# Optimization experiments

Measured on AMD Instinct MI355X. Metric: run time of the kernel, lower is better.

The kernel has to match this reference:

```python
import jax, jax.numpy as jnp
import numpy as np

MAX_SPAN = 255
EPS = 1e-5
B, L, C = 4, 1024, 512
DK, DV, H = 512, 1024, 8
DKH, DVH = DK // H, DV // H


def _bn(x, gamma, beta, axes):
    # Training-mode batch norm: normalize over `axes` per channel.
    m = jnp.mean(x, axis=axes, keepdims=True)
    v = jnp.var(x, axis=axes, keepdims=True)
    return gamma * (x - m) * jax.lax.rsqrt(v + EPS) + beta


def _rel_index(length):
    # distance_matrix[l, m] = m - l + MAX_SPAN - 1, clamped to table range.
    ki = jnp.arange(length)
    d = ki[None, :] - ki[:, None] + (MAX_SPAN - 1)
    return jnp.clip(d, 0, 2 * MAX_SPAN - 2)


def setup_inputs() -> dict:
    key = jax.random.key(0)
    ks = jax.random.split(key, 6)
    std_qkv = DK ** (-0.5)
    return {
        "x": jax.random.normal(ks[0], (B, L, C), jnp.float32),
        "W_qkv": jax.random.normal(ks[1], (C, 2 * DK + DV), jnp.float32) * std_qkv,
        "bn_qkv_gamma": jnp.ones((2 * DK + DV,), jnp.float32),
        "bn_qkv_beta": jnp.zeros((2 * DK + DV,), jnp.float32),
        "bn_sim_gamma": jnp.ones((3, H), jnp.float32),
        "bn_sim_beta": jnp.zeros((3, H), jnp.float32),
        "bn_out_gamma": jnp.ones((2, H, DVH), jnp.float32),
        "bn_out_beta": jnp.zeros((2, H, DVH), jnp.float32),
        "emb_q_rpe": jax.random.normal(ks[2], (2 * MAX_SPAN - 1, DKH), jnp.float32),
        "emb_k_rpe": jax.random.normal(ks[3], (2 * MAX_SPAN - 1, DKH), jnp.float32),
        "emb_v_rpe": jax.random.normal(ks[4], (2 * MAX_SPAN - 1, DVH), jnp.float32),
    }


def reference(x, W_qkv, bn_qkv_gamma, bn_qkv_beta, bn_sim_gamma, bn_sim_beta,
              bn_out_gamma, bn_out_beta, emb_q_rpe, emb_k_rpe, emb_v_rpe):
    b, l, c = x.shape
    rel = _rel_index(l)                                # [L, M] int indices

    qkv = jnp.einsum('blc,cd->bld', x, W_qkv)
    qkv = _bn(qkv, bn_qkv_gamma, bn_qkv_beta, axes=(0, 1))
    q, k, v = jnp.split(qkv, [DK, 2 * DK], axis=-1)
    q = q.reshape(b, l, H, DKH).transpose(0, 2, 1, 3)  # [B,H,L,dk]
    k = k.reshape(b, l, H, DKH).transpose(0, 2, 1, 3)  # [B,H,M,dk]
    v = v.reshape(b, l, H, DVH)                        # [B,M,H,dv]

    q_rpe = emb_q_rpe[rel]                             # [L,M,dk]
    k_rpe = emb_k_rpe[rel]                             # [L,M,dk]
    v_rpe = emb_v_rpe[rel]                             # [L,M,dv]

    sims = jnp.stack([
        jnp.einsum('bhld,bhmd->bhlm', q, k),           # content
        jnp.einsum('bhld,lmd->bhlm', q, q_rpe),        # query rpe
        jnp.einsum('bhmd,lmd->bhlm', k, k_rpe),        # key rpe
    ])                                                 # [3,B,H,L,M]
    sims = _bn(sims, bn_sim_gamma[:, None, :, None, None],
               bn_sim_beta[:, None, :, None, None], axes=(1, 3, 4))
    logits = jnp.sum(sims, axis=0)                     # [B,H,L,M]
    weights = jax.nn.softmax(logits, axis=-1)

    retrieved = jnp.stack([
        jnp.einsum('bhlm,bmhd->bhld', weights, v),     # content
        jnp.einsum('bhlm,lmd->bhld', weights, v_rpe),  # rpe
    ])                                                 # [2,B,H,L,dv]
    retrieved = _bn(retrieved, bn_out_gamma[:, None, :, None, :],
                    bn_out_beta[:, None, :, None, :], axes=(1, 3))
    out = jnp.sum(retrieved, axis=0)                   # [B,H,L,dv]
    out = out.transpose(0, 2, 1, 3).reshape(b, l, DV)
    return out
```

## Files before the change

kernel.cpp:

```cpp
#include <hip/hip_runtime.h>


#define EPSN 1e-5f

#define NWS_QKV   0ul
#define NWS_S     8388608ul
#define NWS_G1    25165824ul
#define NWS_G2    33554432ul
#define NWS_RET   41943040ul
#define NWS_STATS 50331648ul
#define NWS_COLSUM (NWS_STATS)
#define NWS_COLSQ  (NWS_STATS + 2048)
#define NWS_SIMSUM (NWS_STATS + 4096)
#define NWS_SIMSQ  (NWS_STATS + 4120)
#define NWS_OUTSUM (NWS_STATS + 4144)
#define NWS_OUTSQ  (NWS_STATS + 6192)
#define NWS_STATS_N 8240ul
#define NWS_FOLD   (NWS_STATS + NWS_STATS_N)
#define NWS_QSCALE (NWS_FOLD)
#define NWS_QSHIFT (NWS_FOLD + 2048)
#define NWS_SIMA   (NWS_FOLD + 4096)
#define NWS_SIMC   (NWS_FOLD + 4120)
#define NWS_TOTAL_FLOATS (NWS_FOLD + 4128ul)

#define NWS_XHI (NWS_RET)
#define NWS_XLO (NWS_RET + 1048576ul)
#define NWS_WTH (NWS_RET + 2097152ul)
#define NWS_WTL (NWS_RET + 2621440ul)
#define NWS_VB  (NWS_G1)
#define NWS_EVB (NWS_G2)

typedef __attribute__((ext_vector_type(8))) short short8v;
typedef __attribute__((ext_vector_type(4))) float float4v;

__device__ __forceinline__ unsigned short f2bf(float x) {
    union { float f; unsigned int u; } c; c.f = x;
    unsigned int u = c.u + 0x7fffu + ((c.u >> 16) & 1u);
    return (unsigned short)(u >> 16);
}
__device__ __forceinline__ float bf2f(unsigned short x) {
    union { unsigned int u; float f; } c; c.u = ((unsigned int)x) << 16;
    return c.f;
}

__global__ __launch_bounds__(256) void k_prepx(const float* __restrict__ x,
                                               unsigned short* __restrict__ xh,
                                               unsigned short* __restrict__ xl) {
    const size_t e = ((size_t)blockIdx.x * 256 + threadIdx.x) * 8;
    unsigned short th[8], tl[8];
    #pragma unroll
    for (int i = 0; i < 2; ++i) {
        float4 v = *(const float4*)(x + e + i * 4);
        float vv[4] = {v.x, v.y, v.z, v.w};
        #pragma unroll
        for (int j = 0; j < 4; ++j) {
            unsigned short hi = f2bf(vv[j]);
            th[i*4+j] = hi;
            tl[i*4+j] = f2bf(vv[j] - bf2f(hi));
        }
    }
    *(uint4*)(xh + e) = *(uint4*)th;
    *(uint4*)(xl + e) = *(uint4*)tl;
}

__global__ __launch_bounds__(256) void k_prepw(const float* __restrict__ w,
                                               unsigned short* __restrict__ wth,
                                               unsigned short* __restrict__ wtl) {
    __shared__ float ws[64][68];
    const int t = threadIdx.x;
    const int n0 = blockIdx.x * 64;
    const int k0 = blockIdx.y * 64;
    #pragma unroll
    for (int i = 0; i < 4; ++i) {
        int row = (t >> 4) + i * 16;
        int col = (t & 15) * 4;
        float4 v = *(const float4*)(w + (size_t)(k0 + row) * 2048 + n0 + col);
        ws[row][col] = v.x; ws[row][col+1] = v.y; ws[row][col+2] = v.z; ws[row][col+3] = v.w;
    }
    __syncthreads();
    const int n = t >> 2;
    const int kc = (t & 3) * 16;
    unsigned short th[16], tl[16];
    #pragma unroll
    for (int j = 0; j < 16; ++j) {
        float v = ws[kc + j][n];
        unsigned short hi = f2bf(v);
        th[j] = hi; tl[j] = f2bf(v - bf2f(hi));
    }
    size_t base = (size_t)(n0 + n) * 512 + k0 + kc;
    *(uint4*)(wth + base) = *(uint4*)&th[0];
    *(uint4*)(wth + base + 8) = *(uint4*)&th[8];
    *(uint4*)(wtl + base) = *(uint4*)&tl[0];
    *(uint4*)(wtl + base + 8) = *(uint4*)&tl[8];
}

__global__ __launch_bounds__(256) void k_gemm_qkv2(
        const unsigned short* __restrict__ xh, const unsigned short* __restrict__ xl,
        const unsigned short* __restrict__ wth, const unsigned short* __restrict__ wtl,
        float* __restrict__ qkv) {
    __shared__ unsigned short Ah[4096], Al[4096], Bh[4096], Bl[4096];
    const int t = threadIdx.x;
    const int lane = t & 63, w = t >> 6;
    const int n0 = blockIdx.x * 64;
    const int m0 = blockIdx.y * 64;
    const int sr = t >> 2, sc = (t & 3) * 16;
    const int x0 = (sc * 2) ^ ((sr & 7) << 4);
    const int x1 = ((sc * 2) + 16) ^ ((sr & 7) << 4);
    const int fr = lane & 15, kg = lane >> 4;

    float4v acc[4];
    #pragma unroll
    for (int nt = 0; nt < 4; ++nt) { acc[nt][0]=0.f; acc[nt][1]=0.f; acc[nt][2]=0.f; acc[nt][3]=0.f; }

    for (int k0 = 0; k0 < 512; k0 += 64) {
        __syncthreads();
        {
            size_t a = (size_t)(m0 + sr) * 512 + k0 + sc;
            uint4 va0 = *(const uint4*)(xh + a), va1 = *(const uint4*)(xh + a + 8);
            *(uint4*)((char*)Ah + sr * 128 + x0) = va0;
            *(uint4*)((char*)Ah + sr * 128 + x1) = va1;
            uint4 vb0 = *(const uint4*)(xl + a), vb1 = *(const uint4*)(xl + a + 8);
            *(uint4*)((char*)Al + sr * 128 + x0) = vb0;
            *(uint4*)((char*)Al + sr * 128 + x1) = vb1;
            size_t bâ = (size_t)(n0 + sr) * 512 + k0 + sc;
            uint4 vc0 = *(const uint4*)(wth + bâ), vc1 = *(const uint4*)(wth + bâ + 8);
            *(uint4*)((char*)Bh + sr * 128 + x0) = vc0;
            *(uint4*)((char*)Bh + sr * 128 + x1) = vc1;
            uint4 vd0 = *(const uint4*)(wtl + bâ), vd1 = *(const uint4*)(wtl + bâ + 8);
            *(uint4*)((char*)Bl + sr * 128 + x0) = vd0;
            *(uint4*)((char*)Bl + sr * 128 + x1) = vd1;
        }
        __syncthreads();
        #pragma unroll
        for (int ks = 0; ks < 2; ++ks) {
            int arow = w * 16 + fr;
            int aoff = (kg * 16 + ks * 64) ^ ((arow & 7) << 4);
            short8v ah = *(short8v*)((char*)Ah + arow * 128 + aoff);
            short8v al = *(short8v*)((char*)Al + arow * 128 + aoff);
            #pragma unroll
            for (int nt = 0; nt < 4; ++nt) {
                int brow = nt * 16 + fr;
                int boff = (kg * 16 + ks * 64) ^ ((brow & 7) << 4);
                short8v bh = *(short8v*)((char*)Bh + brow * 128 + boff);
                short8v bl = *(short8v*)((char*)Bl + brow * 128 + boff);
                acc[nt] = __builtin_amdgcn_mfma_f32_16x16x32_bf16(ah, bh, acc[nt], 0, 0, 0);
                acc[nt] = __builtin_amdgcn_mfma_f32_16x16x32_bf16(ah, bl, acc[nt], 0, 0, 0);
                acc[nt] = __builtin_amdgcn_mfma_f32_16x16x32_bf16(al, bh, acc[nt], 0, 0, 0);
            }
        }
    }
    const int crow = (lane >> 4) * 4, ccol = lane & 15;
    #pragma unroll
    for (int nt = 0; nt < 4; ++nt)
        #pragma unroll
        for (int j = 0; j < 4; ++j)
            qkv[(size_t)(m0 + w * 16 + crow + j) * 2048 + n0 + nt * 16 + ccol] = acc[nt][j];
}

__global__ __launch_bounds__(256) void k_colstats(const float* __restrict__ src,
                                                  float* __restrict__ sum,
                                                  float* __restrict__ sq) {
    const int ch = blockIdx.x * 256 + threadIdx.x;
    const int r0 = blockIdx.y * 256;
    float s = 0.f, q = 0.f;
    for (int r = 0; r < 256; ++r) {
        float v = src[(size_t)(r0 + r) * 2048 + ch];
        s += v; q += v * v;
    }
    atomicAdd(&sum[ch], s);
    atomicAdd(&sq[ch], q);
}

__global__ __launch_bounds__(256) void k_fold_qkv(const float* __restrict__ sum,
                                                  const float* __restrict__ sq,
                                                  const float* __restrict__ gamma,
                                                  const float* __restrict__ beta,
                                                  float* __restrict__ scale,
                                                  float* __restrict__ shift) {
    const int ch = blockIdx.x * 256 + threadIdx.x;
    float m = sum[ch] * (1.f / 4096.f);
    float v = sq[ch] * (1.f / 4096.f) - m * m;
    float sc = gamma[ch] * rsqrtf(v + EPSN);
    scale[ch] = sc;
    shift[ch] = beta[ch] - sc * m;
}

__global__ void k_fold_sim(const float* __restrict__ simsum,
                           const float* __restrict__ simsq,
                           const float* __restrict__ gamma,
                           const float* __restrict__ beta,
                           float* __restrict__ a_out,
                           float* __restrict__ c_out) {
    __shared__ float part[24];
    const int t = threadIdx.x;
    const float inv = 1.f / (4.f * 1024.f * 1024.f);
    if (t < 24) {
        float m = simsum[t] * inv;
        float v = simsq[t] * inv - m * m;
        float a = gamma[t] * rsqrtf(v + EPSN);
        a_out[t] = a;
        part[t] = beta[t] - a * m;
    }
    __syncthreads();
    if (t < 8) c_out[t] = part[t] + part[8 + t] + part[16 + t];
}

__device__ __forceinline__ float g_mult(int WHICH, int row, int r) {
    int c0, c508, rlo, rhi;
    if (WHICH == 1) {
        c0 = row - 253 > 0 ? row - 253 : 0;
        c508 = 770 - row > 0 ? 770 - row : 0;
        rlo = 254 - row > 1 ? 254 - row : 1;
        rhi = 1277 - row < 507 ? 1277 - row : 507;
    } else {
        c0 = 770 - row > 0 ? 770 - row : 0;
        c508 = row - 253 > 0 ? row - 253 : 0;
        rlo = row - 769 > 1 ? row - 769 : 1;
        rhi = row + 254 < 507 ? row + 254 : 507;
    }
    return (r == 0) ? (float)c0
         : (r == 508) ? (float)c508
         : (r >= rlo && r <= rhi) ? 1.f : 0.f;
}

template<int GM>
__global__ __launch_bounds__(256) void k_gemm_bt(
        const float* __restrict__ qkv,
        const float* __restrict__ qscale, const float* __restrict__ qshift,
        const float* __restrict__ emb,
        unsigned short* __restrict__ outp,
        float* __restrict__ simsum, float* __restrict__ simsq) {
    __shared__ unsigned short Ab[64 * 64];
    __shared__ unsigned short Bb[64 * 64];
    const int t = threadIdx.x;
    const int lane = t & 63, w = t >> 6;
    const int n0 = blockIdx.x * 64;
    const int m0 = blockIdx.y * 64;
    const int z  = blockIdx.z;
    const int sr = t >> 2, sc = (t & 3) * 16;

    {
        int grow = m0 + sr;
        const float* src; int ch;
        if (GM == 0) {
            int b = z >> 3, h = z & 7;
            ch = h * 64 + sc;
            src = qkv + ((size_t)(b * 1024 + grow)) * 2048 + ch;
        } else {
            int zz = grow >> 10, l = grow & 1023;
            int b = zz >> 3, h = zz & 7;
            ch = (GM == 2 ? 512 : 0) + h * 64 + sc;
            src = qkv + ((size_t)(b * 1024 + l)) * 2048 + ch;
        }
        unsigned short tmp[16];
        #pragma unroll
        for (int i = 0; i < 4; ++i) {
            float4 v  = *(const float4*)(src + i * 4);
            float4 s4 = *(const float4*)(qscale + ch + i * 4);
            float4 h4 = *(const float4*)(qshift + ch + i * 4);
            tmp[i*4+0] = f2bf(v.x*s4.x+h4.x); tmp[i*4+1] = f2bf(v.y*s4.y+h4.y);
            tmp[i*4+2] = f2bf(v.z*s4.z+h4.z); tmp[i*4+3] = f2bf(v.w*s4.w+h4.w);
        }
        int x0 = (sc * 2) ^ ((sr & 7) << 4);
        int x1 = ((sc * 2) + 16) ^ ((sr & 7) << 4);
        *(uint4*)((char*)Ab + sr * 128 + x0) = *(uint4*)&tmp[0];
        *(uint4*)((char*)Ab + sr * 128 + x1) = *(uint4*)&tmp[8];
    }
    {
        unsigned short tmp[16];
        if (GM == 0) {
            int b = z >> 3, h = z & 7;
            int ch = 512 + h * 64 + sc;
            const float* src = qkv + ((size_t)(b * 1024 + n0 + sr)) * 2048 + ch;
            #pragma unroll
            for (int i = 0; i < 4; ++i) {
                float4 v  = *(const float4*)(src + i * 4);
                float4 s4 = *(const float4*)(qscale + ch + i * 4);
                float4 h4 = *(const float4*)(qshift + ch + i * 4);
                tmp[i*4+0] = f2bf(v.x*s4.x+h4.x); tmp[i*4+1] = f2bf(v.y*s4.y+h4.y);
                tmp[i*4+2] = f2bf(v.z*s4.z+h4.z); tmp[i*4+3] = f2bf(v.w*s4.w+h4.w);
            }
        } else {
            int r = n0 + sr;
            if (r < 509) {
                const float* src = emb + (size_t)r * 64 + sc;
                #pragma unroll
                for (int i = 0; i < 4; ++i) {
                    float4 v = *(const float4*)(src + i * 4);
                    tmp[i*4+0] = f2bf(v.x); tmp[i*4+1] = f2bf(v.y);
                    tmp[i*4+2] = f2bf(v.z); tmp[i*4+3] = f2bf(v.w);
                }
            } else {
                #pragma unroll
                for (int i = 0; i < 16; ++i) tmp[i] = 0;
            }
        }
        int x0 = (sc * 2) ^ ((sr & 7) << 4);
        int x1 = ((sc * 2) + 16) ^ ((sr & 7) << 4);
        *(uint4*)((char*)Bb + sr * 128 + x0) = *(uint4*)&tmp[0];
        *(uint4*)((char*)Bb + sr * 128 + x1) = *(uint4*)&tmp[8];
    }
    __syncthreads();

    const int fr = lane & 15, kg = lane >> 4;
    float4v acc[4];
    #pragma unroll
    for (int nt = 0; nt < 4; ++nt) { acc[nt][0]=0.f; acc[nt][1]=0.f; acc[nt][2]=0.f; acc[nt][3]=0.f; }
    #pragma unroll
    for (int ks = 0; ks < 2; ++ks) {
        int arow = w * 16 + fr;
        short8v a = *(short8v*)((char*)Ab + arow * 128 +
                                ((kg * 16 + ks * 64) ^ ((arow & 7) << 4)));
        #pragma unroll
        for (int nt = 0; nt < 4; ++nt) {
            int brow = nt * 16 + fr;
            short8v bf = *(short8v*)((char*)Bb + brow * 128 +
                                     ((kg * 16 + ks * 64) ^ ((brow & 7) << 4)));
            acc[nt] = __builtin_amdgcn_mfma_f32_16x16x32_bf16(a, bf, acc[nt], 0, 0, 0);
        }
    }

    const int crow = (lane >> 4) * 4;
    const int ccol = lane & 15;
    size_t base; int ldc;
    if (GM == 0) { base = (((size_t)z * 1024) + m0 + w * 16) * 1024 + n0; ldc = 1024; }
    else         { base = ((size_t)(m0 + w * 16)) * 512 + n0;             ldc = 512;  }
    #pragma unroll
    for (int nt = 0; nt < 4; ++nt)
        #pragma unroll
        for (int j = 0; j < 4; ++j)
            outp[base + (size_t)(crow + j) * ldc + nt * 16 + ccol] = f2bf(acc[nt][j]);

    float s = 0.f, q = 0.f;
    #pragma unroll
    for (int nt = 0; nt < 4; ++nt)
        #pragma unroll
        for (int j = 0; j < 4; ++j) {
            float v = acc[nt][j];
            float mlt;
            if (GM == 0) mlt = 1.f;
            else {
                int row = (m0 + w * 16 + crow + j) & 1023;
                int r = n0 + nt * 16 + ccol;
                mlt = g_mult(GM, row, r);
            }
            s += mlt * v; q += mlt * v * v;
        }
    #pragma unroll
    for (int off = 32; off; off >>= 1) { s += __shfl_xor(s, off); q += __shfl_xor(q, off); }
    __syncthreads();
    float* red = (float*)Ab;
    if (lane == 0) { red[w * 2] = s; red[w * 2 + 1] = q; }
    __syncthreads();
    if (t == 0) {
        float s4 = red[0] + red[2] + red[4] + red[6];
        float q4 = red[1] + red[3] + red[5] + red[7];
        int h = (GM == 0) ? (z & 7) : (((m0 >> 10)) & 7);
        int off0 = (GM == 0) ? 0 : (GM == 1 ? 8 : 16);
        atomicAdd(&simsum[off0 + h], s4);
        atomicAdd(&simsq[off0 + h], q4);
    }
}

__global__ __launch_bounds__(256) void k_logits(
        unsigned short* __restrict__ Sg,
        const unsigned short* __restrict__ G1g,
        const unsigned short* __restrict__ G2g,
        const float* __restrict__ sim_a) {
    const int t = threadIdx.x;
    const int l = blockIdx.x;
    const int z = blockIdx.y;
    const int h = z & 7;
    const float a0c = sim_a[h], a1c = sim_a[8 + h], a2c = sim_a[16 + h];
    const size_t zS = (size_t)z << 20;
    const size_t zG = (size_t)z * 524288;
    const int m = t * 4;
    unsigned short* sp = Sg + zS + (size_t)l * 1024 + m;
    uint2 sv = *(const uint2*)sp;
    const unsigned short* s16 = (const unsigned short*)&sv;
    const unsigned short* g1r = G1g + zG + (size_t)l * 512;
    unsigned short o16[4];
    #pragma unroll
    for (int j = 0; j < 4; ++j) {
        int r = m + j - l + 254;
        int rc = r < 0 ? 0 : (r > 508 ? 508 : r);
        float g1 = bf2f(g1r[rc]);
        float g2 = bf2f(G2g[zG + (size_t)(m + j) * 512 + rc]);
        float lg = a0c * bf2f(s16[j]) + a1c * g1 + a2c * g2;
        o16[j] = f2bf(lg);
    }
    *(uint2*)sp = *(uint2*)o16;
}

__global__ __launch_bounds__(256) void k_prepv(const float* __restrict__ qkv,
                                               const float* __restrict__ qscale,
                                               const float* __restrict__ qshift,
                                               unsigned short* __restrict__ vb) {
    const int row = blockIdx.x;
    const int ch = threadIdx.x * 4;
    float4 v  = *(const float4*)(qkv + (size_t)row * 2048 + 1024 + ch);
    float4 s4 = *(const float4*)(qscale + 1024 + ch);
    float4 h4 = *(const float4*)(qshift + 1024 + ch);
    unsigned short o[4];
    o[0] = f2bf(v.x*s4.x+h4.x); o[1] = f2bf(v.y*s4.y+h4.y);
    o[2] = f2bf(v.z*s4.z+h4.z); o[3] = f2bf(v.w*s4.w+h4.w);
    *(uint2*)(vb + (size_t)row * 1024 + ch) = *(uint2*)o;
}

__global__ __launch_bounds__(256) void k_prepev(const float* __restrict__ ev,
                                                unsigned short* __restrict__ evb) {
    const int e = blockIdx.x * 256 + threadIdx.x;
    const int r = e >> 7, d = e & 127;
    evb[e] = (r < 509) ? f2bf(ev[(size_t)r * 128 + d]) : (unsigned short)0;
}

#define W3_Ws 0
#define W3_Wr 1152
#define W3_V  9472

__global__ __launch_bounds__(256, 4) void k_attn4(
        const unsigned short* __restrict__ Lg,
        const unsigned short* __restrict__ Vb,
        const unsigned short* __restrict__ EVb,
        float* __restrict__ ret) {
    __shared__ unsigned short su[17920];
    const int t = threadIdx.x;
    const int lane = t & 63, wid = t >> 6;
    const int blk = blockIdx.x;
    const int lt = blk & 63;
    const int h  = (blk >> 6) & 7;
    const int b  = blk >> 9;
    const int l0 = lt * 16;
    const int z  = b * 8 + h;
    const size_t zS = (size_t)z << 20;

    {
        unsigned int* wz = (unsigned int*)(su + W3_Wr);
        #pragma unroll
        for (int i = 0; i < 17; ++i) { int idx = t + i * 256; if (idx < 4160) wz[idx] = 0u; }
    }
    float D[4]  = {0.f, 0.f, 0.f, 0.f};
    float e0[4] = {0.f, 0.f, 0.f, 0.f};
    float e1[4] = {0.f, 0.f, 0.f, 0.f};
    float4v accA0, accA1;
    accA0[0]=0.f; accA0[1]=0.f; accA0[2]=0.f; accA0[3]=0.f;
    accA1[0]=0.f; accA1[1]=0.f; accA1[2]=0.f; accA1[3]=0.f;

    const int vm = t >> 2, vd0 = (t & 3) * 32;
    const int fr = lane & 15, kg = lane >> 4;
    const int dbase = wid * 32;
    const size_t vbase = ((size_t)b * 1024) * 1024 + h * 128;

    for (int mt = 0; mt < 16; ++mt) {
        const int m0 = mt * 64;
        __syncthreads();
        uint4 vld[4];
        {
            const unsigned short* src = Vb + vbase + (size_t)(m0 + vm) * 1024 + vd0;
            vld[0] = *(const uint4*)(src);
            vld[1] = *(const uint4*)(src + 8);
            vld[2] = *(const uint4*)(src + 16);
            vld[3] = *(const uint4*)(src + 24);
        }
        #pragma unroll
        for (int rr = 0; rr < 4; ++rr) {
            const int lrow = wid * 4 + rr;
            const int l_g = l0 + lrow;
            const int r = m0 + lane - l_g + 254;
            float wv = __expf(bf2f(Lg[zS + (size_t)l_g * 1024 + m0 + lane]));
            D[rr] += wv;
            bool lo = r <= 0, hi = r >= 508;
            e0[rr] += lo ? wv : 0.f;
            e1[rr] += hi ? wv : 0.f;
            unsigned short hw = f2bf(wv);
            su[W3_Ws + lrow * 72 + lane] = hw;
            if (!lo && !hi) su[W3_Wr + lrow * 520 + r] = hw;
        }
        {
            unsigned short* dst = su + W3_V + vm * 132 + vd0;
            const uint2* vsrc = (const uint2*)vld;
            #pragma unroll
            for (int i = 0; i < 8; ++i) *(uint2*)(dst + i * 4) = vsrc[i];
        }
        __syncthreads();
        #pragma unroll
        for (int ks = 0; ks < 2; ++ks) {
            short8v af = *(const short8v*)(su + W3_Ws + fr * 72 + ks * 32 + kg * 8);
            #pragma unroll
            for (int nt = 0; nt < 2; ++nt) {
                const int d = dbase + nt * 16 + fr;
                const unsigned short* vp = su + W3_V + (ks * 32 + kg * 8) * 132 + d;
                short8v bf;
                bf[0] = (short)vp[0 * 132]; bf[1] = (short)vp[1 * 132];
                bf[2] = (short)vp[2 * 132]; bf[3] = (short)vp[3 * 132];
                bf[4] = (short)vp[4 * 132]; bf[5] = (short)vp[5 * 132];
                bf[6] = (short)vp[6 * 132]; bf[7] = (short)vp[7 * 132];
                if (nt == 0) accA0 = __builtin_amdgcn_mfma_f32_16x16x32_bf16(af, bf, accA0, 0, 0, 0);
                else         accA1 = __builtin_amdgcn_mfma_f32_16x16x32_bf16(af, bf, accA1, 0, 0, 0);
            }
        }
    }

    #pragma unroll
    for (int rr = 0; rr < 4; ++rr) {
        #pragma unroll
        for (int off = 32; off; off >>= 1) {
            D[rr]  += __shfl_xor(D[rr], off);
            e0[rr] += __shfl_xor(e0[rr], off);
            e1[rr] += __shfl_xor(e1[rr], off);
        }
    }
    float* Df = (float*)su;
    __syncthreads();
    if (lane == 0) {
        #pragma unroll
        for (int rr = 0; rr < 4; ++rr) {
            int lrow = wid * 4 + rr;
            Df[lrow] = D[rr];
            su[W3_Wr + lrow * 520 + 0]   = f2bf(e0[rr]);
            su[W3_Wr + lrow * 520 + 508] = f2bf(e1[rr]);
        }
    }
    __syncthreads();

    const int crow = (lane >> 4) * 4, ccol = lane & 15;
    {
        size_t rb = (((size_t)b * 8 + h) * 1024 + l0) * 128;
        #pragma unroll
        for (int j = 0; j < 4; ++j) {
            int row = crow + j;
            float dinv = 1.f / Df[row];
            ret[rb + (size_t)row * 128 + dbase + ccol]      = accA0[j] * dinv;
            ret[rb + (size_t)row * 128 + dbase + 16 + ccol] = accA1[j] * dinv;
        }
    }

    float4v accR0, accR1;
    accR0[0]=0.f; accR0[1]=0.f; accR0[2]=0.f; accR0[3]=0.f;
    accR1[0]=0.f; accR1[1]=0.f; accR1[2]=0.f; accR1[3]=0.f;
    for (int rc = 0; rc < 8; ++rc) {
        __syncthreads();
        {
            const unsigned short* src = EVb + (size_t)(rc * 64 + vm) * 128 + vd0;
            unsigned short* dst = su + W3_V + vm * 132 + vd0;
            uint4 a0 = *(const uint4*)(src);
            uint4 a1 = *(const uint4*)(src + 8);
            uint4 a2 = *(const uint4*)(src + 16);
            uint4 a3 = *(const uint4*)(src + 24);
            uint4 tmp[4] = {a0, a1, a2, a3};
            const uint2* vsrc = (const uint2*)tmp;
            #pragma unroll
            for (int i = 0; i < 8; ++i) *(uint2*)(dst + i * 4) = vsrc[i];
        }
        __syncthreads();
        #pragma unroll
        for (int ks = 0; ks < 2; ++ks) {
            short8v af = *(const short8v*)(su + W3_Wr + fr * 520 + rc * 64 + ks * 32 + kg * 8);
            #pragma unroll
            for (int nt = 0; nt < 2; ++nt) {
                const int d = dbase + nt * 16 + fr;
                const unsigned short* vp = su + W3_V + (ks * 32 + kg * 8) * 132 + d;
                short8v bf;
                bf[0] = (short)vp[0 * 132]; bf[1] = (short)vp[1 * 132];
                bf[2] = (short)vp[2 * 132]; bf[3] = (short)vp[3 * 132];
                bf[4] = (short)vp[4 * 132]; bf[5] = (short)vp[5 * 132];
                bf[6] = (short)vp[6 * 132]; bf[7] = (short)vp[7 * 132];
                if (nt == 0) accR0 = __builtin_amdgcn_mfma_f32_16x16x32_bf16(af, bf, accR0, 0, 0, 0);
                else         accR1 = __builtin_amdgcn_mfma_f32_16x16x32_bf16(af, bf, accR1, 0, 0, 0);
            }
        }
    }
    {
        size_t rb = ((((size_t)1 * 4 + b) * 8 + h) * 1024 + l0) * 128;
        #pragma unroll
        for (int j = 0; j < 4; ++j) {
            int row = crow + j;
            float dinv = 1.f / Df[row];
            ret[rb + (size_t)row * 128 + dbase + ccol]      = accR0[j] * dinv;
            ret[rb + (size_t)row * 128 + dbase + 16 + ccol] = accR1[j] * dinv;
        }
    }
}

__global__ __launch_bounds__(256) void k_outstats(const float* __restrict__ ret,
                                                  float* __restrict__ sum,
                                                  float* __restrict__ sq) {
    const int ch = blockIdx.x * 256 + threadIdx.x;
    const int s = ch >> 10, hd = ch & 1023;
    const int h = hd >> 7, d = hd & 127;
    const int row0 = blockIdx.y * 256;
    float sm_ = 0.f, q = 0.f;
    for (int r = 0; r < 256; ++r) {
        int row = row0 + r;
        int b = row >> 10, l = row & 1023;
        float v = ret[((((size_t)s * 4 + b) * 8 + h) * 1024 + l) * 128 + d];
        sm_ += v; q += v * v;
    }
    atomicAdd(&sum[ch], sm_);
    atomicAdd(&sq[ch], q);
}

__global__ __launch_bounds__(256) void k_final(const float* __restrict__ ret,
                                               const float* __restrict__ osum,
                                               const float* __restrict__ osq,
                                               const float* __restrict__ gamma,
                                               const float* __restrict__ beta,
                                               float* __restrict__ out) {
    const int idx = blockIdx.x * 256 + threadIdx.x;
    const int o = idx * 4;
    const int d = o & 127;
    const int h = (o >> 7) & 7;
    const int l = (o >> 10) & 1023;
    const int b = o >> 20;
    const int ch0 = h * 128 + d;
    const int ch1 = 1024 + ch0;
    float4 r0 = *(const float4*)(ret + ((((size_t)0 * 4 + b) * 8 + h) * 1024 + l) * 128 + d);
    float4 r1 = *(const float4*)(ret + ((((size_t)1 * 4 + b) * 8 + h) * 1024 + l) * 128 + d);
    float4 s0 = *(const float4*)(osum + ch0), q0 = *(const float4*)(osq + ch0);
    float4 s1 = *(const float4*)(osum + ch1), q1 = *(const float4*)(osq + ch1);
    float4 g0 = *(const float4*)(gamma + ch0), b0 = *(const float4*)(beta + ch0);
    float4 g1 = *(const float4*)(gamma + ch1), b1 = *(const float4*)(beta + ch1);
    const float inv = 1.f / 4096.f;
    float4 res;
    {
        float m0 = s0.x*inv, v0 = q0.x*inv - m0*m0, a0 = g0.x*rsqrtf(v0+EPSN);
        float m1 = s1.x*inv, v1 = q1.x*inv - m1*m1, a1 = g1.x*rsqrtf(v1+EPSN);
        res.x = a0*(r0.x-m0)+b0.x + a1*(r1.x-m1)+b1.x;
    }
    {
        float m0 = s0.y*inv, v0 = q0.y*inv - m0*m0, a0 = g0.y*rsqrtf(v0+EPSN);
        float m1 = s1.y*inv, v1 = q1.y*inv - m1*m1, a1 = g1.y*rsqrtf(v1+EPSN);
        res.y = a0*(r0.y-m0)+b0.y + a1*(r1.y-m1)+b1.y;
    }
    {
        float m0 = s0.z*inv, v0 = q0.z*inv - m0*m0, a0 = g0.z*rsqrtf(v0+EPSN);
        float m1 = s1.z*inv, v1 = q1.z*inv - m1*m1, a1 = g1.z*rsqrtf(v1+EPSN);
        res.z = a0*(r0.z-m0)+b0.z + a1*(r1.z-m1)+b1.z;
    }
    {
        float m0 = s0.w*inv, v0 = q0.w*inv - m0*m0, a0 = g0.w*rsqrtf(v0+EPSN);
        float m1 = s1.w*inv, v1 = q1.w*inv - m1*m1, a1 = g1.w*rsqrtf(v1+EPSN);
        res.w = a0*(r0.w-m0)+b0.w + a1*(r1.w-m1)+b1.w;
    }
    *(float4*)(out + o) = res;
}

extern "C" void kernel_launch(void* const* d_in, const int* in_sizes, int n_in,
                              void* d_out, int out_size, void* d_ws, size_t ws_size,
                              hipStream_t stream) {
    const float* x     = (const float*)d_in[0];
    const float* wqkv  = (const float*)d_in[1];
    const float* g_qkv = (const float*)d_in[2];
    const float* b_qkv = (const float*)d_in[3];
    const float* g_sim = (const float*)d_in[4];
    const float* b_sim = (const float*)d_in[5];
    const float* g_out = (const float*)d_in[6];
    const float* b_out = (const float*)d_in[7];
    const float* eq    = (const float*)d_in[8];
    const float* ek    = (const float*)d_in[9];
    const float* ev    = (const float*)d_in[10];
    float* ws  = (float*)d_ws;
    float* out = (float*)d_out;

    if (ws_size < NWS_TOTAL_FLOATS * sizeof(float)) {
        hipMemsetAsync(out, 0, (size_t)out_size * sizeof(float), stream);
        return;
    }

    float* qkv    = ws + NWS_QKV;
    unsigned short* Sg  = (unsigned short*)(ws + NWS_S);
    unsigned short* G1g = (unsigned short*)(ws + NWS_G1);
    unsigned short* G2g = (unsigned short*)(ws + NWS_G2);
    float* ret    = ws + NWS_RET;
    float* colsum = ws + NWS_COLSUM;
    float* colsq  = ws + NWS_COLSQ;
    float* simsum = ws + NWS_SIMSUM;
    float* simsq  = ws + NWS_SIMSQ;
    float* outsum = ws + NWS_OUTSUM;
    float* outsq  = ws + NWS_OUTSQ;
    float* qscale = ws + NWS_QSCALE;
    float* qshift = ws + NWS_QSHIFT;
    float* sim_a  = ws + NWS_SIMA;
    float* sim_c  = ws + NWS_SIMC;
    unsigned short* xh  = (unsigned short*)(ws + NWS_XHI);
    unsigned short* xl  = (unsigned short*)(ws + NWS_XLO);
    unsigned short* wth = (unsigned short*)(ws + NWS_WTH);
    unsigned short* wtl = (unsigned short*)(ws + NWS_WTL);
    unsigned short* vb  = (unsigned short*)(ws + NWS_VB);
    unsigned short* evb = (unsigned short*)(ws + NWS_EVB);
    (void)sim_c;

    hipMemsetAsync(ws + NWS_STATS, 0, NWS_STATS_N * sizeof(float), stream);

    k_prepx<<<dim3(1024), 256, 0, stream>>>(x, xh, xl);
    k_prepw<<<dim3(32, 8), 256, 0, stream>>>(wqkv, wth, wtl);
    k_gemm_qkv2<<<dim3(32, 64), 256, 0, stream>>>(xh, xl, wth, wtl, qkv);

    k_colstats<<<dim3(8, 16), 256, 0, stream>>>(qkv, colsum, colsq);
    k_fold_qkv<<<dim3(8), 256, 0, stream>>>(colsum, colsq, g_qkv, b_qkv, qscale, qshift);

    k_gemm_bt<0><<<dim3(16, 16, 32), 256, 0, stream>>>(qkv, qscale, qshift, eq, Sg, simsum, simsq);
    k_gemm_bt<1><<<dim3(8, 512, 1), 256, 0, stream>>>(qkv, qscale, qshift, eq, G1g, simsum, simsq);
    k_gemm_bt<2><<<dim3(8, 512, 1), 256, 0, stream>>>(qkv, qscale, qshift, ek, G2g, simsum, simsq);

    k_fold_sim<<<dim3(1), 32, 0, stream>>>(simsum, simsq, g_sim, b_sim, sim_a, ws + NWS_SIMC);

    k_logits<<<dim3(1024, 32), 256, 0, stream>>>(Sg, G1g, G2g, sim_a);

    k_prepv<<<dim3(4096), 256, 0, stream>>>(qkv, qscale, qshift, vb);
    k_prepev<<<dim3(256), 256, 0, stream>>>(ev, evb);

    k_attn4<<<dim3(2048), 256, 0, stream>>>(Sg, vb, evb, ret);

    k_outstats<<<dim3(8, 16), 256, 0, stream>>>(ret, outsum, outsq);
    k_final<<<dim3(4096), 256, 0, stream>>>(ret, outsum, outsq, g_out, b_out, out);
}
```

Baseline: 656.0 us.

## Fuse logits combination into attention kernel and pre-transpose V operands

```diff
diff --git a/kernel.cpp b/kernel.cpp
--- a/kernel.cpp
+++ b/kernel.cpp
@@ -27,8 +27,6 @@
 #define NWS_XLO (NWS_RET + 1048576ul)
 #define NWS_WTH (NWS_RET + 2097152ul)
 #define NWS_WTL (NWS_RET + 2621440ul)
-#define NWS_VB  (NWS_G1)
-#define NWS_EVB (NWS_G2)
 
 typedef __attribute__((ext_vector_type(8))) short short8v;
 typedef __attribute__((ext_vector_type(4))) float float4v;
@@ -116,19 +114,15 @@
         __syncthreads();
         {
             size_t a = (size_t)(m0 + sr) * 512 + k0 + sc;
-            uint4 va0 = *(const uint4*)(xh + a), va1 = *(const uint4*)(xh + a + 8);
-            *(uint4*)((char*)Ah + sr * 128 + x0) = va0;
-            *(uint4*)((char*)Ah + sr * 128 + x1) = va1;
-            uint4 vb0 = *(const uint4*)(xl + a), vb1 = *(const uint4*)(xl + a + 8);
-            *(uint4*)((char*)Al + sr * 128 + x0) = vb0;
-            *(uint4*)((char*)Al + sr * 128 + x1) = vb1;
-            size_t bâ = (size_t)(n0 + sr) * 512 + k0 + sc;
-            uint4 vc0 = *(const uint4*)(wth + bâ), vc1 = *(const uint4*)(wth + bâ + 8);
-            *(uint4*)((char*)Bh + sr * 128 + x0) = vc0;
-            *(uint4*)((char*)Bh + sr * 128 + x1) = vc1;
-            uint4 vd0 = *(const uint4*)(wtl + bâ), vd1 = *(const uint4*)(wtl + bâ + 8);
-            *(uint4*)((char*)Bl + sr * 128 + x0) = vd0;
-            *(uint4*)((char*)Bl + sr * 128 + x1) = vd1;
+            *(uint4*)((char*)Ah + sr * 128 + x0) = *(const uint4*)(xh + a);
+            *(uint4*)((char*)Ah + sr * 128 + x1) = *(const uint4*)(xh + a + 8);
+            *(uint4*)((char*)Al + sr * 128 + x0) = *(const uint4*)(xl + a);
+            *(uint4*)((char*)Al + sr * 128 + x1) = *(const uint4*)(xl + a + 8);
+            size_t bb = (size_t)(n0 + sr) * 512 + k0 + sc;
+            *(uint4*)((char*)Bh + sr * 128 + x0) = *(const uint4*)(wth + bb);
+            *(uint4*)((char*)Bh + sr * 128 + x1) = *(const uint4*)(wth + bb + 8);
+            *(uint4*)((char*)Bl + sr * 128 + x0) = *(const uint4*)(wtl + bb);
+            *(uint4*)((char*)Bl + sr * 128 + x1) = *(const uint4*)(wtl + bb + 8);
         }
         __syncthreads();
         #pragma unroll
@@ -203,6 +197,87 @@
     }
     __syncthreads();
     if (t < 8) c_out[t] = part[t] + part[8 + t] + part[16 + t];
+}
+
+__global__ __launch_bounds__(256) void k_prepvT(const float* __restrict__ qkv,
+                                                const float* __restrict__ qscale,
+                                                const float* __restrict__ qshift,
+                                                unsigned short* __restrict__ vbT) {
+    __shared__ unsigned short tb[64 * 130];
+    const int t = threadIdx.x;
+    const int blk = blockIdx.x;
+    const int z = blk >> 4, mt = blk & 15;
+    const int b = z >> 3, h = z & 7;
+    const int m0 = mt * 64;
+    {
+        const int m = t >> 2, dg = (t & 3) * 32;
+        const int ch = 1024 + h * 128 + dg;
+        const float* src = qkv + ((size_t)(b * 1024 + m0 + m)) * 2048 + ch;
+        const float* scp = qscale + ch;
+        const float* shp = qshift + ch;
+        unsigned short* dst = tb + m * 130 + dg;
+        #pragma unroll
+        for (int i = 0; i < 8; ++i) {
+            float4 v  = *(const float4*)(src + i * 4);
+            float4 s4 = *(const float4*)(scp + i * 4);
+            float4 h4 = *(const float4*)(shp + i * 4);
+            uint2 pw;
+            pw.x = (unsigned int)f2bf(v.x*s4.x+h4.x) | ((unsigned int)f2bf(v.y*s4.y+h4.y) << 16);
+            pw.y = (unsigned int)f2bf(v.z*s4.z+h4.z) | ((unsigned int)f2bf(v.w*s4.w+h4.w) << 16);
+            *(uint2*)(dst + i * 4) = pw;
+        }
+    }
+    __syncthreads();
+    {
+        const int d = t >> 1, mo = (t & 1) * 32;
+        unsigned short o[32];
+        #pragma unroll
+        for (int j = 0; j < 32; ++j) o[j] = tb[(mo + j) * 130 + d];
+        unsigned short* dst = vbT + ((size_t)z * 128 + d) * 1024 + m0 + mo;
+        *(uint4*)(dst)      = *(uint4*)&o[0];
+        *(uint4*)(dst + 8)  = *(uint4*)&o[8];
+        *(uint4*)(dst + 16) = *(uint4*)&o[16];
+        *(uint4*)(dst + 24) = *(uint4*)&o[24];
+    }
+}
+
+__global__ __launch_bounds__(256) void k_prepevT(const float* __restrict__ ev,
+                                                 unsigned short* __restrict__ evbT) {
+    __shared__ unsigned short tb[64 * 130];
+    const int t = threadIdx.x;
+    const int r0 = blockIdx.x * 64;
+    {
+        const int r = t >> 2, dg = (t & 3) * 32;
+        const int rr = r0 + r;
+        unsigned short* dst = tb + r * 130 + dg;
+        if (rr < 509) {
+            const float* src = ev + (size_t)rr * 128 + dg;
+            #pragma unroll
+            for (int i = 0; i < 8; ++i) {
+                float4 v = *(const float4*)(src + i * 4);
+                uint2 pw;
+                pw.x = (unsigned int)f2bf(v.x) | ((unsigned int)f2bf(v.y) << 16);
+                pw.y = (unsigned int)f2bf(v.z) | ((unsigned int)f2bf(v.w) << 16);
+                *(uint2*)(dst + i * 4) = pw;
+            }
+        } else {
+            uint2 zz; zz.x = 0u; zz.y = 0u;
+            #pragma unroll
+            for (int i = 0; i < 8; ++i) *(uint2*)(dst + i * 4) = zz;
+        }
+    }
+    __syncthreads();
+    {
+        const int d = t >> 1, mo = (t & 1) * 32;
+        unsigned short o[32];
+        #pragma unroll
+        for (int j = 0; j < 32; ++j) o[j] = tb[(mo + j) * 130 + d];
+        unsigned short* dst = evbT + (size_t)d * 512 + r0 + mo;
+        *(uint4*)(dst)      = *(uint4*)&o[0];
+        *(uint4*)(dst + 8)  = *(uint4*)&o[8];
+        *(uint4*)(dst + 16) = *(uint4*)&o[16];
+        *(uint4*)(dst + 24) = *(uint4*)&o[24];
+    }
 }
 
 __device__ __forceinline__ float g_mult(int WHICH, int row, int r) {
@@ -362,68 +437,20 @@
     }
 }
 
-__global__ __launch_bounds__(256) void k_logits(
-        unsigned short* __restrict__ Sg,
+#define A5_Ws 0
+#define A5_Wr 2304
+#define A5_Vt 10624
+#define A5_G2 19840
+
+__global__ __launch_bounds__(256) void k_attn5(
+        const unsigned short* __restrict__ Sg,
         const unsigned short* __restrict__ G1g,
         const unsigned short* __restrict__ G2g,
-        const float* __restrict__ sim_a) {
-    const int t = threadIdx.x;
-    const int l = blockIdx.x;
-    const int z = blockIdx.y;
-    const int h = z & 7;
-    const float a0c = sim_a[h], a1c = sim_a[8 + h], a2c = sim_a[16 + h];
-    const size_t zS = (size_t)z << 20;
-    const size_t zG = (size_t)z * 524288;
-    const int m = t * 4;
-    unsigned short* sp = Sg + zS + (size_t)l * 1024 + m;
-    uint2 sv = *(const uint2*)sp;
-    const unsigned short* s16 = (const unsigned short*)&sv;
-    const unsigned short* g1r = G1g + zG + (size_t)l * 512;
-    unsigned short o16[4];
-    #pragma unroll
-    for (int j = 0; j < 4; ++j) {
-        int r = m + j - l + 254;
-        int rc = r < 0 ? 0 : (r > 508 ? 508 : r);
-        float g1 = bf2f(g1r[rc]);
-        float g2 = bf2f(G2g[zG + (size_t)(m + j) * 512 + rc]);
-        float lg = a0c * bf2f(s16[j]) + a1c * g1 + a2c * g2;
-        o16[j] = f2bf(lg);
-    }
-    *(uint2*)sp = *(uint2*)o16;
-}
-
-__global__ __launch_bounds__(256) void k_prepv(const float* __restrict__ qkv,
-                                               const float* __restrict__ qscale,
-                                               const float* __restrict__ qshift,
-                                               unsigned short* __restrict__ vb) {
-    const int row = blockIdx.x;
-    const int ch = threadIdx.x * 4;
-    float4 v  = *(const float4*)(qkv + (size_t)row * 2048 + 1024 + ch);
-    float4 s4 = *(const float4*)(qscale + 1024 + ch);
-    float4 h4 = *(const float4*)(qshift + 1024 + ch);
-    unsigned short o[4];
-    o[0] = f2bf(v.x*s4.x+h4.x); o[1] = f2bf(v.y*s4.y+h4.y);
-    o[2] = f2bf(v.z*s4.z+h4.z); o[3] = f2bf(v.w*s4.w+h4.w);
-    *(uint2*)(vb + (size_t)row * 1024 + ch) = *(uint2*)o;
-}
-
-__global__ __launch_bounds__(256) void k_prepev(const float* __restrict__ ev,
-                                                unsigned short* __restrict__ evb) {
-    const int e = blockIdx.x * 256 + threadIdx.x;
-    const int r = e >> 7, d = e & 127;
-    evb[e] = (r < 509) ? f2bf(ev[(size_t)r * 128 + d]) : (unsigned short)0;
-}
-
-#define W3_Ws 0
-#define W3_Wr 1152
-#define W3_V  9472
-
-__global__ __launch_bounds__(256, 4) void k_attn4(
-        const unsigned short* __restrict__ Lg,
-        const unsigned short* __restrict__ Vb,
-        const unsigned short* __restrict__ EVb,
+        const unsigned short* __restrict__ VbT,
+        const unsigned short* __restrict__ EVbT,
+        const float* __restrict__ sim_a,
         float* __restrict__ ret) {
-    __shared__ unsigned short su[17920];
+    __shared__ unsigned short su[20992];
     const int t = threadIdx.x;
     const int lane = t & 63, wid = t >> 6;
     const int blk = blockIdx.x;
@@ -433,9 +460,12 @@
     const int l0 = lt * 16;
     const int z  = b * 8 + h;
     const size_t zS = (size_t)z << 20;
-
-    {
-        unsigned int* wz = (unsigned int*)(su + W3_Wr);
+    const size_t zG = (size_t)z * 524288;
+    const size_t vzb = (size_t)z * 131072;
+    const float a0c = sim_a[h], a1c = sim_a[8 + h], a2c = sim_a[16 + h];
+
+    {
+        unsigned int* wz = (unsigned int*)(su + A5_Wr);
         #pragma unroll
         for (int i = 0; i < 17; ++i) { int idx = t + i * 256; if (idx < 4160) wz[idx] = 0u; }
     }
@@ -446,55 +476,59 @@
     accA0[0]=0.f; accA0[1]=0.f; accA0[2]=0.f; accA0[3]=0.f;
     accA1[0]=0.f; accA1[1]=0.f; accA1[2]=0.f; accA1[3]=0.f;
 
-    const int vm = t >> 2, vd0 = (t & 3) * 32;
+    const int sd = t >> 1, smo = (t & 1) * 32;
+    const int gmm = t >> 2, gj0 = (t & 3) * 4;
     const int fr = lane & 15, kg = lane >> 4;
     const int dbase = wid * 32;
-    const size_t vbase = ((size_t)b * 1024) * 1024 + h * 128;
 
     for (int mt = 0; mt < 16; ++mt) {
         const int m0 = mt * 64;
         __syncthreads();
-        uint4 vld[4];
         {
-            const unsigned short* src = Vb + vbase + (size_t)(m0 + vm) * 1024 + vd0;
-            vld[0] = *(const uint4*)(src);
-            vld[1] = *(const uint4*)(src + 8);
-            vld[2] = *(const uint4*)(src + 16);
-            vld[3] = *(const uint4*)(src + 24);
-        }
+            const unsigned short* src = VbT + vzb + (size_t)sd * 1024 + m0 + smo;
+            unsigned short* dst = su + A5_Vt + sd * 72 + smo;
+            *(uint4*)(dst)      = *(const uint4*)(src);
+            *(uint4*)(dst + 8)  = *(const uint4*)(src + 8);
+            *(uint4*)(dst + 16) = *(const uint4*)(src + 16);
+            *(uint4*)(dst + 24) = *(const uint4*)(src + 24);
+        }
+        {
+            const unsigned short* g = G2g + zG + (size_t)(m0 + gmm) * 512;
+            int rb = m0 + gmm - l0 + 254;
+            #pragma unroll
+            for (int j = 0; j < 4; ++j) {
+                int lr = gj0 + j;
+                int rc = rb - lr; rc = rc < 0 ? 0 : (rc > 508 ? 508 : rc);
+                su[A5_G2 + gmm * 18 + lr] = g[rc];
+            }
+        }
+        __syncthreads();
         #pragma unroll
         for (int rr = 0; rr < 4; ++rr) {
             const int lrow = wid * 4 + rr;
             const int l_g = l0 + lrow;
             const int r = m0 + lane - l_g + 254;
-            float wv = __expf(bf2f(Lg[zS + (size_t)l_g * 1024 + m0 + lane]));
+            const int rc = r < 0 ? 0 : (r > 508 ? 508 : r);
+            float sval = bf2f(Sg[zS + (size_t)l_g * 1024 + m0 + lane]);
+            float g1   = bf2f(G1g[zG + (size_t)l_g * 512 + rc]);
+            float g2   = bf2f(su[A5_G2 + lane * 18 + lrow]);
+            float wv = __expf(a0c * sval + a1c * g1 + a2c * g2);
             D[rr] += wv;
             bool lo = r <= 0, hi = r >= 508;
             e0[rr] += lo ? wv : 0.f;
             e1[rr] += hi ? wv : 0.f;
             unsigned short hw = f2bf(wv);
-            su[W3_Ws + lrow * 72 + lane] = hw;
-            if (!lo && !hi) su[W3_Wr + lrow * 520 + r] = hw;
-        }
-        {
-            unsigned short* dst = su + W3_V + vm * 132 + vd0;
-            const uint2* vsrc = (const uint2*)vld;
-            #pragma unroll
-            for (int i = 0; i < 8; ++i) *(uint2*)(dst + i * 4) = vsrc[i];
+            su[A5_Ws + lrow * 72 + lane] = hw;
+            if (!lo && !hi) su[A5_Wr + lrow * 520 + r] = hw;
         }
         __syncthreads();
         #pragma unroll
         for (int ks = 0; ks < 2; ++ks) {
-            short8v af = *(const short8v*)(su + W3_Ws + fr * 72 + ks * 32 + kg * 8);
+            short8v af = *(const short8v*)(su + A5_Ws + fr * 72 + ks * 32 + kg * 8);
             #pragma unroll
             for (int nt = 0; nt < 2; ++nt) {
                 const int d = dbase + nt * 16 + fr;
-                const unsigned short* vp = su + W3_V + (ks * 32 + kg * 8) * 132 + d;
-                short8v bf;
-                bf[0] = (short)vp[0 * 132]; bf[1] = (short)vp[1 * 132];
-                bf[2] = (short)vp[2 * 132]; bf[3] = (short)vp[3 * 132];
-                bf[4] = (short)vp[4 * 132]; bf[5] = (short)vp[5 * 132];
-                bf[6] = (short)vp[6 * 132]; bf[7] = (short)vp[7 * 132];
+                short8v bf = *(const short8v*)(su + A5_Vt + d * 72 + ks * 32 + kg * 8);
                 if (nt == 0) accA0 = __builtin_amdgcn_mfma_f32_16x16x32_bf16(af, bf, accA0, 0, 0, 0);
                 else         accA1 = __builtin_amdgcn_mfma_f32_16x16x32_bf16(af, bf, accA1, 0, 0, 0);
             }
@@ -517,8 +551,8 @@
         for (int rr = 0; rr < 4; ++rr) {
             int lrow = wid * 4 + rr;
             Df[lrow] = D[rr];
-            su[W3_Wr + lrow * 520 + 0]   = f2bf(e0[rr]);
-            su[W3_Wr + lrow * 520 + 508] = f2bf(e1[rr]);
+            su[A5_Wr + lrow * 520 + 0]   = f2bf(e0[rr]);
+            su[A5_Wr + lrow * 520 + 508] = f2bf(e1[rr]);
         }
     }
     __syncthreads();
@@ -541,30 +575,21 @@
     for (int rc = 0; rc < 8; ++rc) {
         __syncthreads();
         {
-            const unsigned short* src = EVb + (size_t)(rc * 64 + vm) * 128 + vd0;
-            unsigned short* dst = su + W3_V + vm * 132 + vd0;
-            uint4 a0 = *(const uint4*)(src);
-            uint4 a1 = *(const uint4*)(src + 8);
-            uint4 a2 = *(const uint4*)(src + 16);
-            uint4 a3 = *(const uint4*)(src + 24);
-            uint4 tmp[4] = {a0, a1, a2, a3};
-            const uint2* vsrc = (const uint2*)tmp;
-            #pragma unroll
-            for (int i = 0; i < 8; ++i) *(uint2*)(dst + i * 4) = vsrc[i];
+            const unsigned short* src = EVbT + (size_t)sd * 512 + rc * 64 + smo;
+            unsigned short* dst = su + A5_Vt + sd * 72 + smo;
+            *(uint4*)(dst)      = *(const uint4*)(src);
+            *(uint4*)(dst + 8)  = *(const uint4*)(src + 8);
+            *(uint4*)(dst + 16) = *(const uint4*)(src + 16);
+            *(uint4*)(dst + 24) = *(const uint4*)(src + 24);
         }
         __syncthreads();
         #pragma unroll
         for (int ks = 0; ks < 2; ++ks) {
-            short8v af = *(const short8v*)(su + W3_Wr + fr * 520 + rc * 64 + ks * 32 + kg * 8);
+            short8v af = *(const short8v*)(su + A5_Wr + fr * 520 + rc * 64 + ks * 32 + kg * 8);
             #pragma unroll
             for (int nt = 0; nt < 2; ++nt) {
                 const int d = dbase + nt * 16 + fr;
-                const unsigned short* vp = su + W3_V + (ks * 32 + kg * 8) * 132 + d;
-                short8v bf;
-                bf[0] = (short)vp[0 * 132]; bf[1] = (short)vp[1 * 132];
-                bf[2] = (short)vp[2 * 132]; bf[3] = (short)vp[3 * 132];
-                bf[4] = (short)vp[4 * 132]; bf[5] = (short)vp[5 * 132];
-                bf[6] = (short)vp[6 * 132]; bf[7] = (short)vp[7 * 132];
+                short8v bf = *(const short8v*)(su + A5_Vt + d * 72 + ks * 32 + kg * 8);
                 if (nt == 0) accR0 = __builtin_amdgcn_mfma_f32_16x16x32_bf16(af, bf, accR0, 0, 0, 0);
                 else         accR1 = __builtin_amdgcn_mfma_f32_16x16x32_bf16(af, bf, accR1, 0, 0, 0);
             }
@@ -681,14 +706,12 @@
     float* qscale = ws + NWS_QSCALE;
     float* qshift = ws + NWS_QSHIFT;
     float* sim_a  = ws + NWS_SIMA;
-    float* sim_c  = ws + NWS_SIMC;
     unsigned short* xh  = (unsigned short*)(ws + NWS_XHI);
     unsigned short* xl  = (unsigned short*)(ws + NWS_XLO);
     unsigned short* wth = (unsigned short*)(ws + NWS_WTH);
     unsigned short* wtl = (unsigned short*)(ws + NWS_WTL);
-    unsigned short* vb  = (unsigned short*)(ws + NWS_VB);
-    unsigned short* evb = (unsigned short*)(ws + NWS_EVB);
-    (void)sim_c;
+    unsigned short* vbT  = (unsigned short*)out;
+    unsigned short* evbT = (unsigned short*)(out + 2097152);
 
     hipMemsetAsync(ws + NWS_STATS, 0, NWS_STATS_N * sizeof(float), stream);
 
@@ -699,18 +722,16 @@
     k_colstats<<<dim3(8, 16), 256, 0, stream>>>(qkv, colsum, colsq);
     k_fold_qkv<<<dim3(8), 256, 0, stream>>>(colsum, colsq, g_qkv, b_qkv, qscale, qshift);
 
+    k_prepvT<<<dim3(512), 256, 0, stream>>>(qkv, qscale, qshift, vbT);
+    k_prepevT<<<dim3(8), 256, 0, stream>>>(ev, evbT);
+
     k_gemm_bt<0><<<dim3(16, 16, 32), 256, 0, stream>>>(qkv, qscale, qshift, eq, Sg, simsum, simsq);
     k_gemm_bt<1><<<dim3(8, 512, 1), 256, 0, stream>>>(qkv, qscale, qshift, eq, G1g, simsum, simsq);
     k_gemm_bt<2><<<dim3(8, 512, 1), 256, 0, stream>>>(qkv, qscale, qshift, ek, G2g, simsum, simsq);
 
     k_fold_sim<<<dim3(1), 32, 0, stream>>>(simsum, simsq, g_sim, b_sim, sim_a, ws + NWS_SIMC);
 
-    k_logits<<<dim3(1024, 32), 256, 0, stream>>>(Sg, G1g, G2g, sim_a);
-
-    k_prepv<<<dim3(4096), 256, 0, stream>>>(qkv, qscale, qshift, vb);
-    k_prepev<<<dim3(256), 256, 0, stream>>>(ev, evb);
-
-    k_attn4<<<dim3(2048), 256, 0, stream>>>(Sg, vb, evb, ret);
+    k_attn5<<<dim3(2048), 256, 0, stream>>>(Sg, G1g, G2g, vbT, evbT, sim_a, ret);
 
     k_outstats<<<dim3(8, 16), 256, 0, stream>>>(ret, outsum, outsq);
     k_final<<<dim3(4096), 256, 0, stream>>>(ret, outsum, outsq, g_out, b_out, out);
```

New measurement: 559.1 us. 1.17x faster.
